# Performance work log

Hardware: AMD Instinct MI355X
Metric: run time of the kernel (lower is better)

## Reference

```python
import jax, jax.numpy as jnp
import numpy as np

B, L, C, H, W = 2, 32, 128, 32, 32
R_MIN, R_MAX = 0.8, 0.99


def setup_inputs() -> dict:
    key = jax.random.key(0)
    ks = jax.random.split(key, 12)
    x = jax.random.normal(ks[0], (B, L, C, H, W), jnp.float32)
    # LRU initialization exactly as in the torch module
    u1 = jax.random.uniform(ks[1], (C, H), jnp.float32)
    u2 = jax.random.uniform(ks[2], (C, H), jnp.float32)
    nu_log = jnp.log(-0.5 * jnp.log(u1 * (R_MAX**2 - R_MIN**2) + R_MIN**2))
    theta_log = jnp.log(u2 * 2.0 * jnp.pi)
    abs_lam = jnp.exp(-jnp.exp(nu_log))  # |lambda| = exp(-nu)
    gamma_log = jnp.log(jnp.sqrt(1.0 - abs_lam**2))
    params_log = jnp.concatenate([nu_log, theta_log, gamma_log], axis=0)  # [3C, H]
    s = 0.05
    Wb_re = jax.random.normal(ks[3], (C, C), jnp.float32) * s
    Wb_im = jax.random.normal(ks[4], (C, C), jnp.float32) * s
    bb_re = jax.random.normal(ks[5], (C,), jnp.float32) * s
    bb_im = jax.random.normal(ks[6], (C,), jnp.float32) * s
    Wc_re = jax.random.normal(ks[7], (C, C), jnp.float32) * s
    Wc_im = jax.random.normal(ks[8], (C, C), jnp.float32) * s
    bc_re = jax.random.normal(ks[9], (C,), jnp.float32) * s
    bc_im = jax.random.normal(ks[10], (C,), jnp.float32) * s
    ln_w = jnp.ones((C, H, W), jnp.float32)
    ln_b = jnp.zeros((C, H, W), jnp.float32)
    return dict(x=x, params_log=params_log, Wb_re=Wb_re, Wb_im=Wb_im, bb_re=bb_re,
                bb_im=bb_im, Wc_re=Wc_re, Wc_im=Wc_im, bc_re=bc_re, bc_im=bc_im,
                ln_w=ln_w, ln_b=ln_b)


def reference(x, params_log, Wb_re, Wb_im, bb_re, bb_im, Wc_re, Wc_im, bc_re, bc_im, ln_w, ln_b):
    Cn = x.shape[2]
    nu = jnp.exp(params_log[:Cn])           # [C,H]
    theta = jnpp_exp = jnp.exp(params_log[Cn:2 * Cn])
    gamma = jnp.exp(params_log[2 * Cn:])    # [C,H]
    lam = jnp.exp(-nu + 1j * theta)         # [C,H] complex, |lam|<1

    # FFT2 over spatial dims
    h = jnp.fft.fft2(x.astype(jnp.complex64))  # [B,L,C,H,W]
    # complex 1x1 conv proj_B (CxC GEMM per pixel)
    Wb = (Wb_re + 1j * Wb_im).astype(jnp.complex64)
    bb = (bb_re + 1j * bb_im).astype(jnp.complex64)
    h = jnp.einsum('oc,blchw->blohw', Wb, h) + bb[None, None, :, None, None]
    # gamma gating, broadcast over B,L,W
    h = h * gamma[None, None, :, :, None]

    # linear recurrence y_t = lam * y_{t-1} + h_t (pscan), lam constant in t
    lam_b = lam[None, :, :, None]  # [1,C,H,1] broadcasts over [B,C,H,W]
    def step(carry, ht):
        y = lam_b * carry + ht
        return y, y
    h_t = jnp.moveaxis(h, 1, 0)  # [L,B,C,H,W]
    _, ys = jax.lax.scan(step, jnp.zeros_like(h_t[0]), h_t)
    h = jnp.moveaxis(ys, 0, 1)   # [B,L,C,H,W]
    last_hidden_out = h[:, -1:]

    h = jnp.fft.ifft2(h)
    Wc = (Wc_re + 1j * Wc_im).astype(jnp.complex64)
    bc = (bc_re + 1j * bc_im).astype(jnp.complex64)
    h = jnp.einsum('oc,blchw->blohw', Wc, h) + bc[None, None, :, None, None]
    h = h.real  # real cast, dropout is identity in eval

    # LayerNorm over (C,H,W) jointly
    mean = jnp.mean(h, axis=(2, 3, 4), keepdims=True)
    var = jnp.var(h, axis=(2, 3, 4), keepdims=True)
    h = (h - mean) / jnp.sqrt(var + 1e-5) * ln_w + ln_b
    return h + x, last_hidden_out
```

## Files before the change

kernel.cpp:

```cpp
#include <hip/hip_runtime.h>
#include <cstdint>
#include <cstddef>

#define DEVINL __device__ __forceinline__

static constexpr int Bdim = 2, Ldim = 32, Cdim = 128, Hdim = 32, Wdim = 32;
static constexpr int HW  = Hdim * Wdim;
static constexpr int CHW = Cdim * HW;
static constexpr size_t OUT0_ELEMS = (size_t)Bdim * Ldim * CHW;
static constexpr size_t OUT1_CPLX  = (size_t)Bdim * CHW;

typedef __attribute__((ext_vector_type(8))) short short8v;
typedef __attribute__((ext_vector_type(4))) float f32x4;

DEVINL int bitrev5(int v) {
    return ((v&1)<<4) | ((v&2)<<2) | (v&4) | ((v&8)>>2) | ((v&16)>>4);
}
DEVINL unsigned short f2bf(float v) {
    unsigned u = __float_as_uint(v);
    return (unsigned short)((u + 0x7FFFu + ((u >> 16) & 1u)) >> 16);
}
DEVINL void bfsplit(float v, short& hi, short& lo) {
    unsigned short hb = f2bf(v);
    hi = (short)hb;
    float hf = __uint_as_float(((unsigned)hb) << 16);
    lo = (short)f2bf(v - hf);
}
DEVINL unsigned pack2bf(float2 v) {
    return (unsigned)f2bf(v.x) | ((unsigned)f2bf(v.y) << 16);
}
DEVINL float2 unpack2bf(unsigned u) {
    return make_float2(__uint_as_float(u << 16), __uint_as_float(u & 0xFFFF0000u));
}

template<int INV>
DEVINL void fft32_reg(float2 v[32]) {
    constexpr float TC[16] = { 1.0f, 0.980785280f, 0.923879533f, 0.831469612f,
                               0.707106781f, 0.555570233f, 0.382683432f, 0.195090322f,
                               0.0f, -0.195090322f, -0.382683432f, -0.555570233f,
                              -0.707106781f, -0.831469612f, -0.923879533f, -0.980785280f };
    constexpr float TS[16] = { 0.0f, -0.195090322f, -0.382683432f, -0.555570233f,
                              -0.707106781f, -0.831469612f, -0.923879533f, -0.980785280f,
                              -1.0f, -0.980785280f, -0.923879533f, -0.831469612f,
                              -0.707106781f, -0.555570233f, -0.382683432f, -0.195090322f };
#pragma unroll
    for (int st = 0; st < 5; ++st) {
        const int half = 1 << st;
#pragma unroll
        for (int bf = 0; bf < 16; ++bf) {
            const int g = bf >> st;
            const int j = bf & (half - 1);
            const int i0 = (g << (st+1)) + j;
            const float wr = TC[j << (4-st)];
            const float wi = INV ? -TS[j << (4-st)] : TS[j << (4-st)];
            float2 a0 = v[i0], a1 = v[i0+half];
            float tr = wr*a1.x - wi*a1.y;
            float ti = wr*a1.y + wi*a1.x;
            v[i0]      = make_float2(a0.x+tr, a0.y+ti);
            v[i0+half] = make_float2(a0.x-tr, a0.y-ti);
        }
    }
}

__global__ __launch_bounds__(256) void pack_w_kernel(
    const float* __restrict__ Wb_re, const float* __restrict__ Wb_im,
    const float* __restrict__ Wc_re, const float* __restrict__ Wc_im,
    const float* __restrict__ pl,
    short* __restrict__ Apack, float* __restrict__ gamma_tab)
{
    const int gid = blockIdx.x*256 + threadIdx.x;
    if (gid < 4096) {
        const int a2   = gid >> 11;
        const int rem  = gid & 2047;
        const int f    = rem >> 6;
        const int lane = rem & 63;
        const int m  = f >> 2, kc = f & 3;
        const int row = m*16 + (lane & 15);
        const int kbase = kc*32 + ((lane >> 4) << 3);
        short8v hi8, lo8;
#pragma unroll
        for (int j = 0; j < 8; ++j) {
            const int c = kbase + j;
            const float v = a2 ? Wb_im[row*Cdim + c] : Wb_re[row*Cdim + c];
            short h, l; bfsplit(v, h, l);
            hi8[j] = h; lo8[j] = l;
        }
        const size_t off = (size_t)(f*64 + lane)*8;
        const size_t base = (size_t)a2 * 32768;
        *reinterpret_cast<short8v*>(Apack + base + off)         = hi8;
        *reinterpret_cast<short8v*>(Apack + base + 16384 + off) = lo8;
    } else if (gid < 8192) {
        const int rem  = gid - 4096;
        const int f    = rem >> 6;
        const int lane = rem & 63;
        const int m  = f >> 3, kc = f & 7;
        const int row = m*16 + (lane & 15);
        const int kbase = kc*32 + ((lane >> 4) << 3);
        short8v hi8, lo8;
#pragma unroll
        for (int j = 0; j < 8; ++j) {
            const int k = kbase + j;
            const int half = k >> 7;
            const int c = k & 127;
            const float v = half ? -Wc_im[row*Cdim + c] : Wc_re[row*Cdim + c];
            short h, l; bfsplit(v, h, l);
            hi8[j] = h; lo8[j] = l;
        }
        const size_t off = (size_t)(f*64 + lane)*8;
        *reinterpret_cast<short8v*>(Apack + 65536 + off)         = hi8;
        *reinterpret_cast<short8v*>(Apack + 65536 + 32768 + off) = lo8;
    } else {
        const int idx = gid - 8192;
        const int c = idx >> 5, hf = idx & 31;
        gamma_tab[idx] = expf(pl[(2*Cdim + c)*Hdim + hf]);
    }
}

__global__ __launch_bounds__(256) void mix0_spatial_kernel(
    const float* __restrict__ x,
    unsigned* __restrict__ Sout,
    const short* __restrict__ Apack)
{
    __shared__ short Bs[4][4][64][8];
    const int bx = blockIdx.x;
    const int bl = bx >> 4, tt = bx & 15;
    const int t = threadIdx.x;
    const int wv = t >> 6, lane = t & 63;

    const float* src = x + (size_t)bl*CHW + tt*64;
#pragma unroll
    for (int g = 0; g < 4; ++g) {
        const int id = g*256 + t;
        const int hw = id & 63;
        const int co = id >> 6;
        const int kc = co >> 2;
        const int ln = (co & 3)*16 + (hw & 15);
        const int nt4 = hw >> 4;
        short8v b8;
#pragma unroll
        for (int j = 0; j < 8; ++j)
            b8[j] = (short)f2bf(src[(size_t)(co*8 + j)*HW + hw]);
        *reinterpret_cast<short8v*>(&Bs[kc][nt4][ln][0]) = b8;
    }
    __syncthreads();

    f32x4 accRe[2][4];
    f32x4 accIm[2][4];
#pragma unroll
    for (int mi = 0; mi < 2; ++mi)
#pragma unroll
        for (int nt = 0; nt < 4; ++nt) {
            accRe[mi][nt] = (f32x4)(0.0f);
            accIm[mi][nt] = (f32x4)(0.0f);
        }

    const short* Are_hi = Apack;
    const short* Are_lo = Apack + 16384;
    const short* Aim_hi = Apack + 32768;
    const short* Aim_lo = Apack + 49152;

#pragma unroll 2
    for (int kc = 0; kc < 4; ++kc) {
        short8v bh[4];
#pragma unroll
        for (int nt = 0; nt < 4; ++nt)
            bh[nt] = *reinterpret_cast<const short8v*>(&Bs[kc][nt][lane][0]);
#pragma unroll
        for (int mi = 0; mi < 2; ++mi) {
            const int m = wv*2 + mi;
            const size_t off = (size_t)((m*4 + kc)*64 + lane)*8;
            const short8v arh = *reinterpret_cast<const short8v*>(Are_hi + off);
            const short8v arl = *reinterpret_cast<const short8v*>(Are_lo + off);
            const short8v aih = *reinterpret_cast<const short8v*>(Aim_hi + off);
            const short8v ail = *reinterpret_cast<const short8v*>(Aim_lo + off);
#pragma unroll
            for (int nt = 0; nt < 4; ++nt) {
                accRe[mi][nt] = __builtin_amdgcn_mfma_f32_16x16x32_bf16(arh, bh[nt], accRe[mi][nt], 0, 0, 0);
                accRe[mi][nt] = __builtin_amdgcn_mfma_f32_16x16x32_bf16(arl, bh[nt], accRe[mi][nt], 0, 0, 0);
                accIm[mi][nt] = __builtin_amdgcn_mfma_f32_16x16x32_bf16(aih, bh[nt], accIm[mi][nt], 0, 0, 0);
                accIm[mi][nt] = __builtin_amdgcn_mfma_f32_16x16x32_bf16(ail, bh[nt], accIm[mi][nt], 0, 0, 0);
            }
        }
    }

    const int col   = lane & 15;
    const int rbase = (lane >> 4) * 4;
#pragma unroll
    for (int mi = 0; mi < 2; ++mi) {
#pragma unroll
        for (int r = 0; r < 4; ++r) {
            const int o = wv*32 + mi*16 + rbase + r;
#pragma unroll
            for (int nt = 0; nt < 4; ++nt) {
                const int wcol = nt*16 + col;
                float2 rv = make_float2(accRe[mi][nt][r], accIm[mi][nt][r]);
                Sout[(size_t)bl*CHW + (size_t)o*HW + tt*64 + wcol] = pack2bf(rv);
            }
        }
    }
}

__global__ __launch_bounds__(256) void fft_gamma_kernel(
    const unsigned* __restrict__ Hsp,
    unsigned* __restrict__ Hfq,
    const float* __restrict__ gamma_tab,
    const float* __restrict__ bb_re, const float* __restrict__ bb_im)
{
    const int gid = blockIdx.x*256 + threadIdx.x;
    const int w = gid & 31;
    const size_t slice = (size_t)(gid >> 5);
    const int c = (int)(slice & 127);
    const unsigned* src = Hsp + slice*HW + w;
    float2 v[32];
#pragma unroll
    for (int i = 0; i < 32; ++i)
        v[i] = unpack2bf(src[(size_t)bitrev5(i)*Wdim]);
    fft32_reg<0>(v);
    const float br = (w == 0) ? bb_re[c] : 0.0f;
    const float bi = (w == 0) ? bb_im[c] : 0.0f;
    const float* gt = gamma_tab + c*32;
    unsigned* dst = Hfq + slice*HW + w;
#pragma unroll
    for (int hf = 0; hf < 32; ++hf) {
        const float g = gt[hf];
        dst[(size_t)hf*Wdim] = pack2bf(make_float2((v[hf].x + br)*g, (v[hf].y + bi)*g));
    }
}

__global__ __launch_bounds__(256) void ifft_h_bf_kernel(const unsigned* __restrict__ Sin,
                                                        unsigned* __restrict__ Ysp) {
    const int gid = blockIdx.x*256 + threadIdx.x;
    const int w = gid & 31;
    const size_t slice = (size_t)(gid >> 5);
    const unsigned* src = Sin + slice*HW + w;
    float2 v[32];
#pragma unroll
    for (int i = 0; i < 32; ++i)
        v[i] = unpack2bf(src[(size_t)bitrev5(i)*Wdim]);
    fft32_reg<1>(v);
    const float sc = 1.0f / 32.0f;
    unsigned* dst = Ysp + slice*HW + w;
#pragma unroll
    for (int h = 0; h < 32; ++h)
        dst[(size_t)h*Wdim] = pack2bf(make_float2(v[h].x*sc, v[h].y*sc));
}

__global__ __launch_bounds__(256) void mix1_kernel(
    const unsigned* __restrict__ Yin,
    const short* __restrict__ Apack,
    const float* __restrict__ bre,
    unsigned short* __restrict__ outr,
    float2* __restrict__ lnpart)
{
    __shared__ short Bs[8][4][64][8];
    const int bx = blockIdx.x;
    const int bl = bx >> 4, tt = bx & 15;
    const int t = threadIdx.x;
    const int wv = t >> 6, lane = t & 63;

    const unsigned* src = Yin + (size_t)bl*CHW + tt*64;
#pragma unroll
    for (int g = 0; g < 4; ++g) {
        const int id = g*256 + t;
        const int hw = id & 63;
        const int co = id >> 6;
        const int kc = co >> 2;
        const int ln = (co & 3)*16 + (hw & 15);
        const int nt4 = hw >> 4;
        unsigned u[8];
#pragma unroll
        for (int j = 0; j < 8; ++j)
            u[j] = src[(size_t)(co*8 + j)*HW + hw];
        unsigned re[4], im[4];
#pragma unroll
        for (int p = 0; p < 4; ++p) {
            re[p] = (u[2*p] & 0xFFFFu) | (u[2*p+1] << 16);
            im[p] = (u[2*p] >> 16) | (u[2*p+1] & 0xFFFF0000u);
        }
        *reinterpret_cast<uint4*>(&Bs[kc][nt4][ln][0])   = make_uint4(re[0], re[1], re[2], re[3]);
        *reinterpret_cast<uint4*>(&Bs[kc+4][nt4][ln][0]) = make_uint4(im[0], im[1], im[2], im[3]);
    }
    __syncthreads();

    f32x4 acc[2][4];
#pragma unroll
    for (int mi = 0; mi < 2; ++mi)
#pragma unroll
        for (int nt = 0; nt < 4; ++nt) acc[mi][nt] = (f32x4)(0.0f);

    const short* A_hi = Apack + 65536;
    const short* A_lo = Apack + 65536 + 32768;

#pragma unroll 2
    for (int kc = 0; kc < 8; ++kc) {
        short8v bh[4];
#pragma unroll
        for (int nt = 0; nt < 4; ++nt)
            bh[nt] = *reinterpret_cast<const short8v*>(&Bs[kc][nt][lane][0]);
#pragma unroll
        for (int mi = 0; mi < 2; ++mi) {
            const int m = wv*2 + mi;
            const size_t off = (size_t)((m*8 + kc)*64 + lane)*8;
            const short8v arh = *reinterpret_cast<const short8v*>(A_hi + off);
            const short8v arl = *reinterpret_cast<const short8v*>(A_lo + off);
#pragma unroll
            for (int nt = 0; nt < 4; ++nt) {
                acc[mi][nt] = __builtin_amdgcn_mfma_f32_16x16x32_bf16(arh, bh[nt], acc[mi][nt], 0, 0, 0);
                acc[mi][nt] = __builtin_amdgcn_mfma_f32_16x16x32_bf16(arl, bh[nt], acc[mi][nt], 0, 0, 0);
            }
        }
    }

    const int col   = lane & 15;
    const int rbase = (lane >> 4) * 4;
    float lns = 0.f, lnq = 0.f;
#pragma unroll
    for (int mi = 0; mi < 2; ++mi) {
#pragma unroll
        for (int r = 0; r < 4; ++r) {
            const int o = wv*32 + mi*16 + rbase + r;
            const float br = bre[o];
#pragma unroll
            for (int nt = 0; nt < 4; ++nt) {
                const int wcol = nt*16 + col;
                const float v = acc[mi][nt][r] + br;
                outr[(size_t)bl*CHW + (size_t)o*HW + tt*64 + wcol] = f2bf(v);
                lns += v; lnq += v*v;
            }
        }
    }
#pragma unroll
    for (int off = 32; off > 0; off >>= 1) {
        lns += __shfl_down(lns, off);
        lnq += __shfl_down(lnq, off);
    }
    __shared__ float2 red[4];
    if (lane == 0) red[wv] = make_float2(lns, lnq);
    __syncthreads();
    if (t == 0) {
        float2 a = red[0], b2 = red[1], c2 = red[2], d = red[3];
        lnpart[bx] = make_float2(a.x + b2.x + c2.x + d.x, a.y + b2.y + c2.y + d.y);
    }
}

template<int CPLX>
__global__ __launch_bounds__(256) void scan_fftw_kernel(
    unsigned* __restrict__ Hf2, const float* __restrict__ pl, float* __restrict__ out1)
{
    const int idx = blockIdx.x*256 + threadIdx.x;
    const int b   = idx >> 17;
    const int chw = idx & (CHW - 1);
    const int c   = chw >> 10;
    const int h   = (chw >> 5) & 31;
    const float nu = expf(pl[c*Hdim + h]);
    const float th = expf(pl[(Cdim + c)*Hdim + h]);
    const float rr = expf(-nu);
    const float lr = rr * cosf(th);
    const float li = rr * sinf(th);
    float2 y = make_float2(0.f, 0.f);
    const size_t basei = (size_t)b * Ldim * CHW + chw;
#pragma unroll 4
    for (int l = 0; l < Ldim; ++l) {
        float2 hv = unpack2bf(Hf2[basei + (size_t)l*CHW]);
        float yr = fmaf(lr, y.x, fmaf(-li, y.y, hv.x));
        float yi = fmaf(lr, y.y, fmaf( li, y.x, hv.y));
        y = make_float2(yr, yi);
        Hf2[basei + (size_t)l*CHW] = pack2bf(y);
    }
    const int a = threadIdx.x & 31;
    float2 v;
    v.x = __shfl(y.x, bitrev5(a), 32);
    v.y = __shfl(y.y, bitrev5(a), 32);
#pragma unroll
    for (int st = 0; st < 5; ++st) {
        const int half = 1 << st;
        const int j = a & (half - 1);
        const float ang = -6.283185307179586f * (float)(j << (4 - st)) / 32.0f;
        float wi, wr;
        __sincosf(ang, &wi, &wr);
        float2 p;
        p.x = __shfl_xor(v.x, half, 32);
        p.y = __shfl_xor(v.y, half, 32);
        const bool top = (a & half) == 0;
        const float2 a1 = top ? p : v;
        const float2 a0 = top ? v : p;
        const float tr = wr*a1.x - wi*a1.y;
        const float ti = wr*a1.y + wi*a1.x;
        v.x = top ? a0.x + tr : a0.x - tr;
        v.y = top ? a0.y + ti : a0.y - ti;
    }
    const size_t row = (size_t)(idx >> 5);
    if (CPLX) {
        reinterpret_cast<float2*>(out1)[row*32 + a] = v;
    } else {
        out1[row*32 + a] = v.x;
    }
}

__global__ __launch_bounds__(64) void ln_finish_kernel(const float2* __restrict__ lnpart,
                                                       float2* __restrict__ stats) {
    const int bl = blockIdx.x;
    const int t = threadIdx.x;
    float s = 0.f, sq = 0.f;
    if (t < 16) { float2 v = lnpart[bl*16 + t]; s = v.x; sq = v.y; }
#pragma unroll
    for (int off = 8; off > 0; off >>= 1) {
        s  += __shfl_down(s, off);
        sq += __shfl_down(sq, off);
    }
    if (t == 0) {
        const float invN = 1.0f / (float)CHW;
        float mean = s * invN;
        float var  = sq * invN - mean*mean;
        stats[bl] = make_float2(mean, rsqrtf(var + 1e-5f));
    }
}

__global__ __launch_bounds__(256) void ln_apply_kernel(
    float* __restrict__ out0, const unsigned short* __restrict__ hpre,
    const float* __restrict__ x,
    const float* __restrict__ lnw, const float* __restrict__ lnb,
    const float2* __restrict__ stats)
{
    const int idx4 = blockIdx.x*256 + threadIdx.x;
    const int i = idx4 * 4;
    const int bl = i >> 17;
    const int chw4 = (i & (CHW - 1)) >> 2;
    const float2 st = stats[bl];
    const uint2 hu = reinterpret_cast<const uint2*>(hpre)[idx4];
    float4 h;
    h.x = __uint_as_float(hu.x << 16);
    h.y = __uint_as_float(hu.x & 0xFFFF0000u);
    h.z = __uint_as_float(hu.y << 16);
    h.w = __uint_as_float(hu.y & 0xFFFF0000u);
    float4 xv = reinterpret_cast<const float4*>(x)[idx4];
    float4 w  = reinterpret_cast<const float4*>(lnw)[chw4];
    float4 bb = reinterpret_cast<const float4*>(lnb)[chw4];
    const float m = st.x, rs = st.y;
    float4 r;
    r.x = fmaf((h.x - m)*rs, w.x, bb.x) + xv.x;
    r.y = fmaf((h.y - m)*rs, w.y, bb.y) + xv.y;
    r.z = fmaf((h.z - m)*rs, w.z, bb.z) + xv.z;
    r.w = fmaf((h.w - m)*rs, w.w, bb.w) + xv.w;
    reinterpret_cast<float4*>(out0)[idx4] = r;
}

extern "C" void kernel_launch(void* const* d_in, const int* in_sizes, int n_in,
                              void* d_out, int out_size, void* d_ws, size_t ws_size,
                              hipStream_t stream)
{
    const float* x     = (const float*)d_in[0];
    const float* pl    = (const float*)d_in[1];
    const float* Wb_re = (const float*)d_in[2];
    const float* Wb_im = (const float*)d_in[3];
    const float* bb_re = (const float*)d_in[4];
    const float* bb_im = (const float*)d_in[5];
    const float* Wc_re = (const float*)d_in[6];
    const float* Wc_im = (const float*)d_in[7];
    const float* bc_re = (const float*)d_in[8];
    const float* bc_im = (const float*)d_in[9];
    const float* ln_w  = (const float*)d_in[10];
    const float* ln_b  = (const float*)d_in[11];
    (void)bc_im;

    float* out0 = (float*)d_out;
    float* out1 = out0 + OUT0_ELEMS;

    char* ws = (char*)d_ws;
    unsigned*       bufA    = (unsigned*)       ws;
    unsigned*       bufB    = (unsigned*)       (ws + 33554432);
    unsigned short* out0pre = (unsigned short*) (ws + 67108864);
    short*          Apack   = (short*)          (ws + 83886080);
    float*          gtab    = (float*)          (ws + 84148224);
    float2*         lnpart  = (float2*)         (ws + 84164608);
    float2*         stats   = (float2*)         (ws + 84172800);

    const bool interleaved = ((size_t)out_size >= OUT0_ELEMS + 2*OUT1_CPLX);

    pack_w_kernel<<<48, 256, 0, stream>>>(Wb_re, Wb_im, Wc_re, Wc_im, pl, Apack, gtab);
    mix0_spatial_kernel<<<1024, 256, 0, stream>>>(x, bufA, Apack);
    fft_gamma_kernel<<<1024, 256, 0, stream>>>(bufA, bufB, gtab, bb_re, bb_im);
    if (interleaved)
        scan_fftw_kernel<1><<<1024, 256, 0, stream>>>(bufB, pl, out1);
    else
        scan_fftw_kernel<0><<<1024, 256, 0, stream>>>(bufB, pl, out1);
    ifft_h_bf_kernel<<<1024, 256, 0, stream>>>(bufB, bufA);
    mix1_kernel<<<1024, 256, 0, stream>>>(bufA, Apack, bc_re, out0pre, lnpart);
    ln_finish_kernel<<<64, 64, 0, stream>>>(lnpart, stats);
    ln_apply_kernel<<<8192, 256, 0, stream>>>(out0, out0pre, x, ln_w, ln_b, stats);
}
```

Before: 97.65 us.

## Fuse output mix, LayerNorm stats and apply into one cooperative kernel

Replaces the mix1, ln_finish and ln_apply kernels with a single cooperative kernel. It computes the Wc GEMM, reduces per-block LayerNorm partials, does a grid-wide sync, then normalises straight from registers and writes the final output. This removes the bf16 intermediate round trip through global memory and two kernel launches. It needs all 1024 blocks co-resident (launch bounds 256,4), and the grid sync adds cost. A fallback path folds the stats finish into the apply kernel.

```diff
diff --git a/kernel.cpp b/kernel.cpp
--- a/kernel.cpp
+++ b/kernel.cpp
@@ -1,6 +1,9 @@
 #include <hip/hip_runtime.h>
+#include <hip/hip_cooperative_groups.h>
 #include <cstdint>
 #include <cstddef>
+
+namespace cg = cooperative_groups;
 
 #define DEVINL __device__ __forceinline__
 
@@ -243,104 +246,6 @@
 #pragma unroll
     for (int h = 0; h < 32; ++h)
         dst[(size_t)h*Wdim] = pack2bf(make_float2(v[h].x*sc, v[h].y*sc));
-}
-
-__global__ __launch_bounds__(256) void mix1_kernel(
-    const unsigned* __restrict__ Yin,
-    const short* __restrict__ Apack,
-    const float* __restrict__ bre,
-    unsigned short* __restrict__ outr,
-    float2* __restrict__ lnpart)
-{
-    __shared__ short Bs[8][4][64][8];
-    const int bx = blockIdx.x;
-    const int bl = bx >> 4, tt = bx & 15;
-    const int t = threadIdx.x;
-    const int wv = t >> 6, lane = t & 63;
-
-    const unsigned* src = Yin + (size_t)bl*CHW + tt*64;
-#pragma unroll
-    for (int g = 0; g < 4; ++g) {
-        const int id = g*256 + t;
-        const int hw = id & 63;
-        const int co = id >> 6;
-        const int kc = co >> 2;
-        const int ln = (co & 3)*16 + (hw & 15);
-        const int nt4 = hw >> 4;
-        unsigned u[8];
-#pragma unroll
-        for (int j = 0; j < 8; ++j)
-            u[j] = src[(size_t)(co*8 + j)*HW + hw];
-        unsigned re[4], im[4];
-#pragma unroll
-        for (int p = 0; p < 4; ++p) {
-            re[p] = (u[2*p] & 0xFFFFu) | (u[2*p+1] << 16);
-            im[p] = (u[2*p] >> 16) | (u[2*p+1] & 0xFFFF0000u);
-        }
-        *reinterpret_cast<uint4*>(&Bs[kc][nt4][ln][0])   = make_uint4(re[0], re[1], re[2], re[3]);
-        *reinterpret_cast<uint4*>(&Bs[kc+4][nt4][ln][0]) = make_uint4(im[0], im[1], im[2], im[3]);
-    }
-    __syncthreads();
-
-    f32x4 acc[2][4];
-#pragma unroll
-    for (int mi = 0; mi < 2; ++mi)
-#pragma unroll
-        for (int nt = 0; nt < 4; ++nt) acc[mi][nt] = (f32x4)(0.0f);
-
-    const short* A_hi = Apack + 65536;
-    const short* A_lo = Apack + 65536 + 32768;
-
-#pragma unroll 2
-    for (int kc = 0; kc < 8; ++kc) {
-        short8v bh[4];
-#pragma unroll
-        for (int nt = 0; nt < 4; ++nt)
-            bh[nt] = *reinterpret_cast<const short8v*>(&Bs[kc][nt][lane][0]);
-#pragma unroll
-        for (int mi = 0; mi < 2; ++mi) {
-            const int m = wv*2 + mi;
-            const size_t off = (size_t)((m*8 + kc)*64 + lane)*8;
-            const short8v arh = *reinterpret_cast<const short8v*>(A_hi + off);
-            const short8v arl = *reinterpret_cast<const short8v*>(A_lo + off);
-#pragma unroll
-            for (int nt = 0; nt < 4; ++nt) {
-                acc[mi][nt] = __builtin_amdgcn_mfma_f32_16x16x32_bf16(arh, bh[nt], acc[mi][nt], 0, 0, 0);
-                acc[mi][nt] = __builtin_amdgcn_mfma_f32_16x16x32_bf16(arl, bh[nt], acc[mi][nt], 0, 0, 0);
-            }
-        }
-    }
-
-    const int col   = lane & 15;
-    const int rbase = (lane >> 4) * 4;
-    float lns = 0.f, lnq = 0.f;
-#pragma unroll
-    for (int mi = 0; mi < 2; ++mi) {
-#pragma unroll
-        for (int r = 0; r < 4; ++r) {
-            const int o = wv*32 + mi*16 + rbase + r;
-            const float br = bre[o];
-#pragma unroll
-            for (int nt = 0; nt < 4; ++nt) {
-                const int wcol = nt*16 + col;
-                const float v = acc[mi][nt][r] + br;
-                outr[(size_t)bl*CHW + (size_t)o*HW + tt*64 + wcol] = f2bf(v);
-                lns += v; lnq += v*v;
-            }
-        }
-    }
-#pragma unroll
-    for (int off = 32; off > 0; off >>= 1) {
-        lns += __shfl_down(lns, off);
-        lnq += __shfl_down(lnq, off);
-    }
-    __shared__ float2 red[4];
-    if (lane == 0) red[wv] = make_float2(lns, lnq);
-    __syncthreads();
-    if (t == 0) {
-        float2 a = red[0], b2 = red[1], c2 = red[2], d = red[3];
-        lnpart[bx] = make_float2(a.x + b2.x + c2.x + d.x, a.y + b2.y + c2.y + d.y);
-    }
 }
 
 template<int CPLX>
@@ -397,36 +302,272 @@
     }
 }
 
-__global__ __launch_bounds__(64) void ln_finish_kernel(const float2* __restrict__ lnpart,
-                                                       float2* __restrict__ stats) {
-    const int bl = blockIdx.x;
+__global__ __launch_bounds__(256, 4) void mix1_ln_coop_kernel(
+    const unsigned* __restrict__ Yin,
+    const short* __restrict__ Apack,
+    const float* __restrict__ bre,
+    const float* __restrict__ x,
+    const float* __restrict__ lnw, const float* __restrict__ lnb,
+    float* __restrict__ out0,
+    float2* __restrict__ lnpart)
+{
+    __shared__ short Bs[8][4][64][8];
+    const int bx = blockIdx.x;
+    const int bl = bx >> 4, tt = bx & 15;
     const int t = threadIdx.x;
-    float s = 0.f, sq = 0.f;
-    if (t < 16) { float2 v = lnpart[bl*16 + t]; s = v.x; sq = v.y; }
-#pragma unroll
-    for (int off = 8; off > 0; off >>= 1) {
-        s  += __shfl_down(s, off);
-        sq += __shfl_down(sq, off);
-    }
+    const int wv = t >> 6, lane = t & 63;
+
+    const unsigned* src = Yin + (size_t)bl*CHW + tt*64;
+#pragma unroll
+    for (int g = 0; g < 4; ++g) {
+        const int id = g*256 + t;
+        const int hw = id & 63;
+        const int co = id >> 6;
+        const int kc = co >> 2;
+        const int ln = (co & 3)*16 + (hw & 15);
+        const int nt4 = hw >> 4;
+        unsigned u[8];
+#pragma unroll
+        for (int j = 0; j < 8; ++j)
+            u[j] = src[(size_t)(co*8 + j)*HW + hw];
+        unsigned re[4], im[4];
+#pragma unroll
+        for (int p = 0; p < 4; ++p) {
+            re[p] = (u[2*p] & 0xFFFFu) | (u[2*p+1] << 16);
+            im[p] = (u[2*p] >> 16) | (u[2*p+1] & 0xFFFF0000u);
+        }
+        *reinterpret_cast<uint4*>(&Bs[kc][nt4][ln][0])   = make_uint4(re[0], re[1], re[2], re[3]);
+        *reinterpret_cast<uint4*>(&Bs[kc+4][nt4][ln][0]) = make_uint4(im[0], im[1], im[2], im[3]);
+    }
+    __syncthreads();
+
+    f32x4 acc[2][4];
+#pragma unroll
+    for (int mi = 0; mi < 2; ++mi)
+#pragma unroll
+        for (int nt = 0; nt < 4; ++nt) acc[mi][nt] = (f32x4)(0.0f);
+
+    const short* A_hi = Apack + 65536;
+    const short* A_lo = Apack + 65536 + 32768;
+
+#pragma unroll 2
+    for (int kc = 0; kc < 8; ++kc) {
+        short8v bh[4];
+#pragma unroll
+        for (int nt = 0; nt < 4; ++nt)
+            bh[nt] = *reinterpret_cast<const short8v*>(&Bs[kc][nt][lane][0]);
+#pragma unroll
+        for (int mi = 0; mi < 2; ++mi) {
+            const int m = wv*2 + mi;
+            const size_t off = (size_t)((m*8 + kc)*64 + lane)*8;
+            const short8v arh = *reinterpret_cast<const short8v*>(A_hi + off);
+            const short8v arl = *reinterpret_cast<const short8v*>(A_lo + off);
+#pragma unroll
+            for (int nt = 0; nt < 4; ++nt) {
+                acc[mi][nt] = __builtin_amdgcn_mfma_f32_16x16x32_bf16(arh, bh[nt], acc[mi][nt], 0, 0, 0);
+                acc[mi][nt] = __builtin_amdgcn_mfma_f32_16x16x32_bf16(arl, bh[nt], acc[mi][nt], 0, 0, 0);
+            }
+        }
+    }
+
+    const int col   = lane & 15;
+    const int rbase = (lane >> 4) * 4;
+    float lns = 0.f, lnq = 0.f;
+#pragma unroll
+    for (int mi = 0; mi < 2; ++mi) {
+#pragma unroll
+        for (int r = 0; r < 4; ++r) {
+            const int o = wv*32 + mi*16 + rbase + r;
+            const float br = bre[o];
+#pragma unroll
+            for (int nt = 0; nt < 4; ++nt) {
+                const float v = acc[mi][nt][r] + br;
+                acc[mi][nt][r] = v;
+                lns += v; lnq += v*v;
+            }
+        }
+    }
+#pragma unroll
+    for (int off = 32; off > 0; off >>= 1) {
+        lns += __shfl_down(lns, off);
+        lnq += __shfl_down(lnq, off);
+    }
+    __shared__ float2 red[4];
+    if (lane == 0) red[wv] = make_float2(lns, lnq);
+    __syncthreads();
     if (t == 0) {
-        const float invN = 1.0f / (float)CHW;
-        float mean = s * invN;
-        float var  = sq * invN - mean*mean;
-        stats[bl] = make_float2(mean, rsqrtf(var + 1e-5f));
-    }
-}
-
-__global__ __launch_bounds__(256) void ln_apply_kernel(
+        float2 a = red[0], b2 = red[1], c2 = red[2], d = red[3];
+        lnpart[bx] = make_float2(a.x + b2.x + c2.x + d.x, a.y + b2.y + c2.y + d.y);
+    }
+    __threadfence();
+
+    cg::this_grid().sync();
+
+    __shared__ float2 mstat;
+    if (t < 64) {
+        float s = 0.f, sq = 0.f;
+        if (t < 16) { float2 v = lnpart[bl*16 + t]; s = v.x; sq = v.y; }
+#pragma unroll
+        for (int off = 8; off > 0; off >>= 1) {
+            s  += __shfl_down(s, off);
+            sq += __shfl_down(sq, off);
+        }
+        if (t == 0) {
+            const float invN = 1.0f / (float)CHW;
+            const float mean = s * invN;
+            const float var  = sq * invN - mean*mean;
+            mstat = make_float2(mean, rsqrtf(var + 1e-5f));
+        }
+    }
+    __syncthreads();
+    const float m  = mstat.x;
+    const float rs = mstat.y;
+
+#pragma unroll
+    for (int mi = 0; mi < 2; ++mi) {
+#pragma unroll
+        for (int r = 0; r < 4; ++r) {
+            const int o = wv*32 + mi*16 + rbase + r;
+#pragma unroll
+            for (int nt = 0; nt < 4; ++nt) {
+                const int wcol = nt*16 + col;
+                const size_t cidx = (size_t)o*HW + tt*64 + wcol;
+                const size_t gidx = (size_t)bl*CHW + cidx;
+                const float v = acc[mi][nt][r];
+                out0[gidx] = fmaf((v - m)*rs, lnw[cidx], lnb[cidx]) + x[gidx];
+            }
+        }
+    }
+}
+
+__global__ __launch_bounds__(256) void mix1_kernel(
+    const unsigned* __restrict__ Yin,
+    const short* __restrict__ Apack,
+    const float* __restrict__ bre,
+    unsigned short* __restrict__ outr,
+    float2* __restrict__ lnpart)
+{
+    __shared__ short Bs[8][4][64][8];
+    const int bx = blockIdx.x;
+    const int bl = bx >> 4, tt = bx & 15;
+    const int t = threadIdx.x;
+    const int wv = t >> 6, lane = t & 63;
+
+    const unsigned* src = Yin + (size_t)bl*CHW + tt*64;
+#pragma unroll
+    for (int g = 0; g < 4; ++g) {
+        const int id = g*256 + t;
+        const int hw = id & 63;
+        const int co = id >> 6;
+        const int kc = co >> 2;
+        const int ln = (co & 3)*16 + (hw & 15);
+        const int nt4 = hw >> 4;
+        unsigned u[8];
+#pragma unroll
+        for (int j = 0; j < 8; ++j)
+            u[j] = src[(size_t)(co*8 + j)*HW + hw];
+        unsigned re[4], im[4];
+#pragma unroll
+        for (int p = 0; p < 4; ++p) {
+            re[p] = (u[2*p] & 0xFFFFu) | (u[2*p+1] << 16);
+            im[p] = (u[2*p] >> 16) | (u[2*p+1] & 0xFFFF0000u);
+        }
+        *reinterpret_cast<uint4*>(&Bs[kc][nt4][ln][0])   = make_uint4(re[0], re[1], re[2], re[3]);
+        *reinterpret_cast<uint4*>(&Bs[kc+4][nt4][ln][0]) = make_uint4(im[0], im[1], im[2], im[3]);
+    }
+    __syncthreads();
+
+    f32x4 acc[2][4];
+#pragma unroll
+    for (int mi = 0; mi < 2; ++mi)
+#pragma unroll
+        for (int nt = 0; nt < 4; ++nt) acc[mi][nt] = (f32x4)(0.0f);
+
+    const short* A_hi = Apack + 65536;
+    const short* A_lo = Apack + 65536 + 32768;
+
+#pragma unroll 2
+    for (int kc = 0; kc < 8; ++kc) {
+        short8v bh[4];
+#pragma unroll
+        for (int nt = 0; nt < 4; ++nt)
+            bh[nt] = *reinterpret_cast<const short8v*>(&Bs[kc][nt][lane][0]);
+#pragma unroll
+        for (int mi = 0; mi < 2; ++mi) {
+            const int m = wv*2 + mi;
+            const size_t off = (size_t)((m*8 + kc)*64 + lane)*8;
+            const short8v arh = *reinterpret_cast<const short8v*>(A_hi + off);
+            const short8v arl = *reinterpret_cast<const short8v*>(A_lo + off);
+#pragma unroll
+            for (int nt = 0; nt < 4; ++nt) {
+                acc[mi][nt] = __builtin_amdgcn_mfma_f32_16x16x32_bf16(arh, bh[nt], acc[mi][nt], 0, 0, 0);
+                acc[mi][nt] = __builtin_amdgcn_mfma_f32_16x16x32_bf16(arl, bh[nt], acc[mi][nt], 0, 0, 0);
+            }
+        }
+    }
+
+    const int col   = lane & 15;
+    const int rbase = (lane >> 4) * 4;
+    float lns = 0.f, lnq = 0.f;
+#pragma unroll
+    for (int mi = 0; mi < 2; ++mi) {
+#pragma unroll
+        for (int r = 0; r < 4; ++r) {
+            const int o = wv*32 + mi*16 + rbase + r;
+            const float br = bre[o];
+#pragma unroll
+            for (int nt = 0; nt < 4; ++nt) {
+                const int wcol = nt*16 + col;
+                const float v = acc[mi][nt][r] + br;
+                outr[(size_t)bl*CHW + (size_t)o*HW + tt*64 + wcol] = f2bf(v);
+                lns += v; lnq += v*v;
+            }
+        }
+    }
+#pragma unroll
+    for (int off = 32; off > 0; off >>= 1) {
+        lns += __shfl_down(lns, off);
+        lnq += __shfl_down(lnq, off);
+    }
+    __shared__ float2 red[4];
+    if (lane == 0) red[wv] = make_float2(lns, lnq);
+    __syncthreads();
+    if (t == 0) {
+        float2 a = red[0], b2 = red[1], c2 = red[2], d = red[3];
+        lnpart[bx] = make_float2(a.x + b2.x + c2.x + d.x, a.y + b2.y + c2.y + d.y);
+    }
+}
+
+__global__ __launch_bounds__(256) void ln_apply2_kernel(
     float* __restrict__ out0, const unsigned short* __restrict__ hpre,
     const float* __restrict__ x,
     const float* __restrict__ lnw, const float* __restrict__ lnb,
-    const float2* __restrict__ stats)
+    const float2* __restrict__ lnpart)
 {
     const int idx4 = blockIdx.x*256 + threadIdx.x;
     const int i = idx4 * 4;
     const int bl = i >> 17;
+    __shared__ float2 mstat;
+    const int t = threadIdx.x;
+    if (t < 64) {
+        float s = 0.f, sq = 0.f;
+        if (t < 16) { float2 v = lnpart[bl*16 + t]; s = v.x; sq = v.y; }
+#pragma unroll
+        for (int off = 8; off > 0; off >>= 1) {
+            s  += __shfl_down(s, off);
+            sq += __shfl_down(sq, off);
+        }
+        if (t == 0) {
+            const float invN = 1.0f / (float)CHW;
+            const float mean = s * invN;
+            const float var  = sq * invN - mean*mean;
+            mstat = make_float2(mean, rsqrtf(var + 1e-5f));
+        }
+    }
+    __syncthreads();
+    const float m = mstat.x, rs = mstat.y;
+
     const int chw4 = (i & (CHW - 1)) >> 2;
-    const float2 st = stats[bl];
     const uint2 hu = reinterpret_cast<const uint2*>(hpre)[idx4];
     float4 h;
     h.x = __uint_as_float(hu.x << 16);
@@ -436,7 +577,6 @@
     float4 xv = reinterpret_cast<const float4*>(x)[idx4];
     float4 w  = reinterpret_cast<const float4*>(lnw)[chw4];
     float4 bb = reinterpret_cast<const float4*>(lnb)[chw4];
-    const float m = st.x, rs = st.y;
     float4 r;
     r.x = fmaf((h.x - m)*rs, w.x, bb.x) + xv.x;
     r.y = fmaf((h.y - m)*rs, w.y, bb.y) + xv.y;
@@ -473,7 +613,6 @@
     short*          Apack   = (short*)          (ws + 83886080);
     float*          gtab    = (float*)          (ws + 84148224);
     float2*         lnpart  = (float2*)         (ws + 84164608);
-    float2*         stats   = (float2*)         (ws + 84172800);
 
     const bool interleaved = ((size_t)out_size >= OUT0_ELEMS + 2*OUT1_CPLX);
 
@@ -485,7 +624,23 @@
     else
         scan_fftw_kernel<0><<<1024, 256, 0, stream>>>(bufB, pl, out1);
     ifft_h_bf_kernel<<<1024, 256, 0, stream>>>(bufB, bufA);
-    mix1_kernel<<<1024, 256, 0, stream>>>(bufA, Apack, bc_re, out0pre, lnpart);
-    ln_finish_kernel<<<64, 64, 0, stream>>>(lnpart, stats);
-    ln_apply_kernel<<<8192, 256, 0, stream>>>(out0, out0pre, x, ln_w, ln_b, stats);
-}
+
+    {
+        const unsigned* yinArg = bufA;
+        const short*    apArg  = Apack;
+        const float*    brArg  = bc_re;
+        const float*    xArg   = x;
+        const float*    lwArg  = ln_w;
+        const float*    lbArg  = ln_b;
+        float*          o0Arg  = out0;
+        float2*         lpArg  = lnpart;
+        void* args[] = { (void*)&yinArg, (void*)&apArg, (void*)&brArg, (void*)&xArg,
+                         (void*)&lwArg, (void*)&lbArg, (void*)&o0Arg, (void*)&lpArg };
+        hipError_t err = hipLaunchCooperativeKernel(
+            (const void*)mix1_ln_coop_kernel, dim3(1024), dim3(256), args, 0, stream);
+        if (err != hipSuccess) {
+            mix1_kernel<<<1024, 256, 0, stream>>>(bufA, Apack, bc_re, out0pre, lnpart);
+            ln_apply2_kernel<<<8192, 256, 0, stream>>>(out0, out0pre, x, ln_w, ln_b, lnpart);
+        }
+    }
+}
```

Result: slower. 202.7 us (+107.6%).
